# Kernel tuning notes

Measured on AMD Instinct MI355X. Metric: run time of the kernel, lower is better.

Reference implementation:

```python
import jax, jax.numpy as jnp
import numpy as np

HEADS = 4
DIM_HEAD = 32
DIM = 128
HIDDEN = HEADS * DIM_HEAD  # 128


def setup_inputs() -> dict:
    key = jax.random.key(0)
    k1, k2, k3, k4 = jax.random.split(key, 4)
    B, C, H, W = 8, DIM, 128, 128
    x = jax.random.normal(k1, (B, C, H, W), dtype=jnp.float32)
    # 1x1 conv weights stored as [out_ch, in_ch] (kernel dims squeezed)
    w_qkv = jax.random.normal(k2, (3 * HIDDEN, DIM), dtype=jnp.float32) * (1.0 / np.sqrt(DIM))
    w_out = jax.random.normal(k3, (DIM, HIDDEN), dtype=jnp.float32) * (1.0 / np.sqrt(HIDDEN))
    b_out = jax.random.normal(k4, (DIM,), dtype=jnp.float32) * 0.01
    return {"x": x, "w_qkv": w_qkv, "w_out": w_out, "b_out": b_out}


def reference(x, w_qkv, w_out, b_out):
    b, c, h, w = x.shape
    n = h * w
    # 1x1 conv == per-pixel matmul over channels
    qkv = jnp.einsum('bchw,oc->bohw', x, w_qkv)            # [b, 3*HIDDEN, h, w]
    # channel layout: (qkv, heads, dim_head)
    qkv = qkv.reshape(b, 3, HEADS, DIM_HEAD, n)            # [b, 3, H, d, n]
    q, k, v = qkv[:, 0], qkv[:, 1], qkv[:, 2]
    k = jax.nn.softmax(k, axis=-1)                         # softmax over spatial n
    context = jnp.einsum('bhdn,bhen->bhde', k, v)          # [b, H, d, d] (tiny)
    out = jnp.einsum('bhde,bhdn->bhen', context, q)        # [b, H, d, n]
    out = out.reshape(b, HIDDEN, h, w)
    y = jnp.einsum('bchw,oc->bohw', out, w_out) + b_out[None, :, None, None]
    return y
```

## Files before the change

kernel.cpp:

```cpp
#include <hip/hip_runtime.h>
#include <math.h>

#define C_ 128
#define N_ 16384

#define WS_Z    0
#define WS_CTX  1024
#define WS_BMAT 33792
#define WS_A    164864
#define WS_PCTX 295936
#define WS_PZ   (WS_PCTX + 1024*4096)
#define WS_END  (WS_PZ + 512*128)

typedef __attribute__((ext_vector_type(8))) short bf16x8;
typedef __attribute__((ext_vector_type(4))) float f32x4;
typedef __attribute__((ext_vector_type(4))) unsigned int u32x4;
typedef __attribute__((ext_vector_type(2))) unsigned int u32x2;

__device__ __forceinline__ unsigned int pkbf(float a, float b) {
  unsigned int r;
  asm("v_cvt_pk_bf16_f32 %0, %1, %2" : "=v"(r) : "v"(a), "v"(b));
  return r;
}

__device__ __forceinline__ bf16x8 make_frag(float4 u, float4 v) {
  u32x4 q = {pkbf(u.x, u.y), pkbf(u.z, u.w), pkbf(v.x, v.y), pkbf(v.z, v.w)};
  return *(bf16x8*)&q;
}

__device__ __forceinline__ bf16x8 lds_frag16(const unsigned short* p) {
  u32x4 q = *(const u32x4*)p;
  return *(bf16x8*)&q;
}

__device__ __forceinline__ void load4(const float* p, float* o) {
  float4 v = *(const float4*)p;
  o[0] = v.x; o[1] = v.y; o[2] = v.z; o[3] = v.w;
}

__device__ __forceinline__ void* xsa(void* base, int row, int col_bytes) {
  return (void*)((char*)base + row * 272 + (col_bytes ^ (((row >> 4) & 3) << 4)));
}

template<bool ATOMIC>
__global__ __launch_bounds__(512, 2) void k1_kv_ctx(const float* __restrict__ x,
                                                    const float* __restrict__ wqkv,
                                                    float* __restrict__ ws) {
  __shared__ __attribute__((aligned(16))) unsigned short xs[64][136];
  __shared__ __attribute__((aligned(16))) unsigned short ekv[2][128][72];
  const int tid  = threadIdx.x;
  const int wave = tid >> 6;
  const int l15  = tid & 15;
  const int l4   = (tid >> 4) & 3;
  const int b    = blockIdx.y;
  const int j    = blockIdx.x;
  const int h    = wave & 3;
  const int t    = wave >> 2;
  const int kvrow0 = h * 32 + t * 128;
  const float* xb = x + (size_t)b * ((size_t)C_ * N_);

  const int sn4 = tid & 15;
  const int scq = tid >> 4;

  bf16x8 wf[2][4];
  #pragma unroll
  for (int mi = 0; mi < 2; ++mi)
    #pragma unroll
    for (int ki = 0; ki < 4; ++ki) {
      const float* p = wqkv + (size_t)(128 + kvrow0 + mi * 16 + l15) * C_ + ki * 32 + l4 * 8;
      wf[mi][ki] = make_frag(*(const float4*)p, *(const float4*)(p + 4));
    }

  {
    float va[4][4];
    #pragma unroll
    for (int r = 0; r < 4; ++r)
      load4(xb + (size_t)(scq * 4 + r) * N_ + j * 256 + sn4 * 4, va[r]);
    #pragma unroll
    for (int i = 0; i < 4; ++i) {
      u32x2 w = {pkbf(va[0][i], va[1][i]), pkbf(va[2][i], va[3][i])};
      *(u32x2*)xsa(xs, sn4 * 4 + i, scq * 8) = w;
    }
  }
  __syncthreads();

  const f32x4 z4 = {0.f, 0.f, 0.f, 0.f};
  f32x4 ctxacc[2][2];
  #pragma unroll
  for (int i = 0; i < 2; ++i)
    #pragma unroll
    for (int jj = 0; jj < 2; ++jj) ctxacc[i][jj] = z4;
  float zacc[2] = {0.f, 0.f};

  for (int st = 0; st < 4; ++st) {
    float pf[4][4];
    if (st < 3) {
      const int nbn = j * 256 + (st + 1) * 64;
      #pragma unroll
      for (int r = 0; r < 4; ++r)
        load4(xb + (size_t)(scq * 4 + r) * N_ + nbn + sn4 * 4, pf[r]);
    }

    #pragma unroll
    for (int half = 0; half < 2; ++half) {
      f32x4 acc[2][2];
      #pragma unroll
      for (int a = 0; a < 2; ++a)
        #pragma unroll
        for (int m = 0; m < 2; ++m) acc[a][m] = z4;
      #pragma unroll
      for (int ki = 0; ki < 4; ++ki) {
        bf16x8 bfr[2];
        #pragma unroll
        for (int ni2 = 0; ni2 < 2; ++ni2)
          bfr[ni2] = lds_frag16((const unsigned short*)
              xsa(xs, half * 32 + ni2 * 16 + l15, ki * 64 + l4 * 16));
        #pragma unroll
        for (int ni2 = 0; ni2 < 2; ++ni2)
          #pragma unroll
          for (int mi = 0; mi < 2; ++mi)
            acc[ni2][mi] = __builtin_amdgcn_mfma_f32_16x16x32_bf16(
                bfr[ni2], wf[mi][ki], acc[ni2][mi], 0, 0, 0);
      }
      #pragma unroll
      for (int ni2 = 0; ni2 < 2; ++ni2)
        #pragma unroll
        for (int mi = 0; mi < 2; ++mi) {
          float e0, e1, e2, e3;
          if (t == 0) {
            e0 = __expf(acc[ni2][mi][0]); e1 = __expf(acc[ni2][mi][1]);
            e2 = __expf(acc[ni2][mi][2]); e3 = __expf(acc[ni2][mi][3]);
            zacc[mi] += (e0 + e1) + (e2 + e3);
          } else {
            e0 = acc[ni2][mi][0]; e1 = acc[ni2][mi][1];
            e2 = acc[ni2][mi][2]; e3 = acc[ni2][mi][3];
          }
          u32x2 w = {pkbf(e0, e1), pkbf(e2, e3)};
          *(u32x2*)&ekv[t][h * 32 + mi * 16 + l15][(half * 2 + ni2) * 16 + l4 * 4] = w;
        }
    }
    __syncthreads();

    {
      bf16x8 af2[2], bv2[2];
      #pragma unroll
      for (int m2 = 0; m2 < 2; ++m2)
        af2[m2] = lds_frag16(&ekv[0][h * 32 + m2 * 16 + l15][t * 32 + l4 * 8]);
      #pragma unroll
      for (int n2 = 0; n2 < 2; ++n2)
        bv2[n2] = lds_frag16(&ekv[1][h * 32 + n2 * 16 + l15][t * 32 + l4 * 8]);
      #pragma unroll
      for (int m2 = 0; m2 < 2; ++m2)
        #pragma unroll
        for (int n2 = 0; n2 < 2; ++n2)
          ctxacc[m2][n2] = __builtin_amdgcn_mfma_f32_16x16x32_bf16(
              af2[m2], bv2[n2], ctxacc[m2][n2], 0, 0, 0);
    }

    if (st < 3) {
      #pragma unroll
      for (int i = 0; i < 4; ++i) {
        u32x2 w = {pkbf(pf[0][i], pf[1][i]), pkbf(pf[2][i], pf[3][i])};
        *(u32x2*)xsa(xs, sn4 * 4 + i, scq * 8) = w;
      }
    }
    __syncthreads();
  }

  if (!ATOMIC) {
    float* ps = ws + WS_PCTX + (size_t)((b * 64 + j) * 2 + t) * 4096 + h * 1024;
    #pragma unroll
    for (int m2 = 0; m2 < 2; ++m2)
      #pragma unroll
      for (int n2 = 0; n2 < 2; ++n2)
        #pragma unroll
        for (int r = 0; r < 4; ++r)
          ps[(m2 * 16 + l4 * 4 + r) * 32 + n2 * 16 + l15] = ctxacc[m2][n2][r];
  } else {
    float* ctx = ws + WS_CTX + (size_t)(b * 4 + h) * 1024;
    #pragma unroll
    for (int m2 = 0; m2 < 2; ++m2)
      #pragma unroll
      for (int n2 = 0; n2 < 2; ++n2)
        #pragma unroll
        for (int r = 0; r < 4; ++r)
          atomicAdd(&ctx[(m2 * 16 + l4 * 4 + r) * 32 + n2 * 16 + l15],
                    ctxacc[m2][n2][r]);
  }
  if (t == 0) {
    #pragma unroll
    for (int mi = 0; mi < 2; ++mi) {
      float z = zacc[mi];
      z += __shfl_xor(z, 16);
      z += __shfl_xor(z, 32);
      if ((tid & 48) == 0) {
        int row = h * 32 + mi * 16 + l15;
        if (!ATOMIC)
          ws[WS_PZ + (size_t)(b * 64 + j) * 128 + row] = z;
        else
          atomicAdd(&ws[WS_Z + b * 128 + row], z);
      }
    }
  }
}

__global__ __launch_bounds__(256) void k1c(float* __restrict__ ws) {
  __shared__ float4 part[4][64];
  const int tid = threadIdx.x;
  const int eq = blockIdx.x;
  const int h  = blockIdx.y;
  const int b  = blockIdx.z;
  const int f4 = tid & 63;
  const int p  = tid >> 6;

  const float* base = ws + WS_PCTX + (size_t)(b * 128) * 4096
                         + h * 1024 + eq * 256 + f4 * 4;
  float4 s = {0.f, 0.f, 0.f, 0.f};
  #pragma unroll 8
  for (int q = 0; q < 32; ++q) {
    float4 v = *(const float4*)(base + (size_t)(p * 32 + q) * 4096);
    s.x += v.x; s.y += v.y; s.z += v.z; s.w += v.w;
  }
  part[p][f4] = s;

  if (eq == 0 && tid < 32) {
    const float* pz = ws + WS_PZ + (size_t)(b * 64) * 128 + h * 32 + tid;
    float z = 0.f;
    #pragma unroll 8
    for (int q = 0; q < 64; ++q) z += pz[(size_t)q * 128];
    ws[WS_Z + b * 128 + h * 32 + tid] = z;
  }
  __syncthreads();

  if (tid < 64) {
    float4 a = part[0][tid], c = part[1][tid], d = part[2][tid], e = part[3][tid];
    float4 o;
    o.x = (a.x + c.x) + (d.x + e.x);
    o.y = (a.y + c.y) + (d.y + e.y);
    o.z = (a.z + c.z) + (d.z + e.z);
    o.w = (a.w + c.w) + (d.w + e.w);
    *(float4*)(ws + WS_CTX + (size_t)(b * 4 + h) * 1024 + eq * 256 + tid * 4) = o;
  }
}

__global__ __launch_bounds__(256) void k2(const float* __restrict__ w_qkv,
                                          const float* __restrict__ w_out,
                                          float* __restrict__ ws) {
  __shared__ float bs[128][132];
  __shared__ float wqs[32][128];
  __shared__ float wos[32][132];
  __shared__ float cn[32][33];
  const int tid = threadIdx.x;
  const int oq = blockIdx.x, b = blockIdx.y;

  for (int h = 0; h < 4; ++h) {
    if (h) __syncthreads();
    const float* Z   = ws + WS_Z + b * 128 + h * 32;
    const float* ctx = ws + WS_CTX + ((b * 4 + h) * 32) * 32;
    #pragma unroll
    for (int k = 0; k < 4; ++k) {
      int idx = tid + k * 256;
      int d = idx >> 5, e = idx & 31;
      cn[d][e] = ctx[d * 32 + e] / Z[d];
    }
    #pragma unroll
    for (int k = 0; k < 4; ++k) {
      int idx = tid + k * 256;
      int d = idx >> 5, f4 = idx & 31;
      *(float4*)&wqs[d][f4 * 4] = *(const float4*)(w_qkv + (h * 32 + d) * 128 + f4 * 4);
    }
    __syncthreads();
    const int e = tid >> 3, cs = (tid & 7) * 16;
    float s[16];
    #pragma unroll
    for (int jj = 0; jj < 16; ++jj) s[jj] = 0.f;
    for (int d = 0; d < 32; ++d) {
      float v = cn[d][e];
      #pragma unroll
      for (int jj = 0; jj < 16; ++jj) s[jj] = fmaf(v, wqs[d][cs + jj], s[jj]);
    }
    #pragma unroll
    for (int jj = 0; jj < 16; ++jj) bs[h * 32 + e][cs + jj] = s[jj];
  }

  __syncthreads();
  #pragma unroll
  for (int k = 0; k < 4; ++k) {
    int idx = tid + k * 256;
    int r = idx >> 5, f4 = idx & 31;
    *(float4*)&wos[r][f4 * 4] = *(const float4*)(w_out + (oq * 32 + r) * 128 + f4 * 4);
  }
  __syncthreads();
  const int ol = tid >> 3, cq = (tid & 7) * 16;
  float s[16];
  #pragma unroll
  for (int jj = 0; jj < 16; ++jj) s[jj] = 0.f;
  for (int eg = 0; eg < 128; ++eg) {
    float w = wos[ol][eg];
    #pragma unroll
    for (int jj = 0; jj < 16; ++jj) s[jj] = fmaf(w, bs[eg][cq + jj], s[jj]);
  }
  float* A = ws + WS_A + ((size_t)b * 128 + oq * 32 + ol) * 128;
  #pragma unroll
  for (int jj = 0; jj < 16; ++jj) A[cq + jj] = s[jj];
}

__global__ __launch_bounds__(256, 2) void k3(const float* __restrict__ x,
                                             const float* __restrict__ bout,
                                             const float* __restrict__ ws,
                                             float* __restrict__ y) {
  __shared__ __attribute__((aligned(16))) unsigned short xs2[2][64][136];
  const int tid  = threadIdx.x;
  const int wave = tid >> 6;
  const int l15  = tid & 15;
  const int l4   = (tid >> 4) & 3;
  const int b    = blockIdx.y;
  const int n0   = blockIdx.x * 128;
  const float* xb = x + (size_t)b * ((size_t)C_ * N_);
  const float* A  = ws + WS_A + (size_t)b * 128 * 128;

  bf16x8 af[2][4];
  #pragma unroll
  for (int mi = 0; mi < 2; ++mi)
    #pragma unroll
    for (int ki = 0; ki < 4; ++ki) {
      const float* p = A + (size_t)(wave * 32 + mi * 16 + l15) * 128 + ki * 32 + l4 * 8;
      af[mi][ki] = make_frag(*(const float4*)p, *(const float4*)(p + 4));
    }
  float bias[2];
  #pragma unroll
  for (int mi = 0; mi < 2; ++mi) bias[mi] = bout[wave * 32 + mi * 16 + l15];

  #pragma unroll
  for (int it = 0; it < 2; ++it) {
    int idx = tid + it * 256;
    int n4 = idx & 15, cq = idx >> 4;
    float va[4][4];
    #pragma unroll
    for (int r = 0; r < 4; ++r)
      load4(xb + (size_t)(cq * 4 + r) * N_ + n0 + n4 * 4, va[r]);
    #pragma unroll
    for (int i = 0; i < 4; ++i) {
      u32x2 w = {pkbf(va[0][i], va[1][i]), pkbf(va[2][i], va[3][i])};
      *(u32x2*)xsa(&xs2[0][0][0], n4 * 4 + i, cq * 8) = w;
    }
  }
  __syncthreads();

  const f32x4 z4 = {0.f, 0.f, 0.f, 0.f};
  float* yb = y + (size_t)b * ((size_t)128 * N_);

  #pragma unroll
  for (int st = 0; st < 2; ++st) {
    const int nb = n0 + st * 64;
    f32x4 acc[4][2];
    #pragma unroll
    for (int ni = 0; ni < 4; ++ni)
      #pragma unroll
      for (int mi = 0; mi < 2; ++mi) acc[ni][mi] = z4;
    #pragma unroll
    for (int ki = 0; ki < 4; ++ki) {
      bf16x8 bfr[4];
      #pragma unroll
      for (int ni = 0; ni < 4; ++ni)
        bfr[ni] = lds_frag16((const unsigned short*)
            xsa(&xs2[st][0][0], ni * 16 + l15, ki * 64 + l4 * 16));
      #pragma unroll
      for (int ni = 0; ni < 4; ++ni)
        #pragma unroll
        for (int mi = 0; mi < 2; ++mi)
          acc[ni][mi] = __builtin_amdgcn_mfma_f32_16x16x32_bf16(
              bfr[ni], af[mi][ki], acc[ni][mi], 0, 0, 0);
    }

    if (st == 0) {
      #pragma unroll
      for (int it = 0; it < 2; ++it) {
        int idx = tid + it * 256;
        int n4 = idx & 15, cq = idx >> 4;
        float va[4][4];
        #pragma unroll
        for (int r = 0; r < 4; ++r)
          load4(xb + (size_t)(cq * 4 + r) * N_ + n0 + 64 + n4 * 4, va[r]);
        #pragma unroll
        for (int i = 0; i < 4; ++i) {
          u32x2 w = {pkbf(va[0][i], va[1][i]), pkbf(va[2][i], va[3][i])};
          *(u32x2*)xsa(&xs2[1][0][0], n4 * 4 + i, cq * 8) = w;
        }
      }
    }

    #pragma unroll
    for (int ni = 0; ni < 4; ++ni)
      #pragma unroll
      for (int mi = 0; mi < 2; ++mi) {
        float4 o;
        o.x = acc[ni][mi][0] + bias[mi];
        o.y = acc[ni][mi][1] + bias[mi];
        o.z = acc[ni][mi][2] + bias[mi];
        o.w = acc[ni][mi][3] + bias[mi];
        *(float4*)(yb + (size_t)(wave * 32 + mi * 16 + l15) * N_ + nb + ni * 16 + l4 * 4) = o;
      }

    if (st == 0) __syncthreads();
  }
}

extern "C" void kernel_launch(void* const* d_in, const int* in_sizes, int n_in,
                              void* d_out, int out_size, void* d_ws, size_t ws_size,
                              hipStream_t stream) {
  const float* x     = (const float*)d_in[0];
  const float* w_qkv = (const float*)d_in[1];
  const float* w_out = (const float*)d_in[2];
  const float* b_out = (const float*)d_in[3];
  float* y  = (float*)d_out;
  float* ws = (float*)d_ws;

  const bool partial = ws_size >= (size_t)WS_END * sizeof(float);
  if (partial) {
    k1_kv_ctx<false><<<dim3(64, 8), 512, 0, stream>>>(x, w_qkv, ws);
    k1c<<<dim3(4, 4, 8), 256, 0, stream>>>(ws);
  } else {
    hipMemsetAsync(ws, 0, (1024 + 32768) * sizeof(float), stream);
    k1_kv_ctx<true><<<dim3(64, 8), 512, 0, stream>>>(x, w_qkv, ws);
  }
  k2<<<dim3(4, 8), 256, 0, stream>>>(w_qkv, w_out, ws);
  k3<<<dim3(128, 8), 256, 0, stream>>>(x, b_out, ws, y);
}
```

Measured before the change: 77.84 us.

## Restructure output projection kernel to 512 threads with double-buffered x pipeline

```diff
diff --git a/kernel.cpp b/kernel.cpp
--- a/kernel.cpp
+++ b/kernel.cpp
@@ -115,12 +115,14 @@
         for (int ni2 = 0; ni2 < 2; ++ni2)
           bfr[ni2] = lds_frag16((const unsigned short*)
               xsa(xs, half * 32 + ni2 * 16 + l15, ki * 64 + l4 * 16));
+        __builtin_amdgcn_s_setprio(1);
         #pragma unroll
         for (int ni2 = 0; ni2 < 2; ++ni2)
           #pragma unroll
           for (int mi = 0; mi < 2; ++mi)
             acc[ni2][mi] = __builtin_amdgcn_mfma_f32_16x16x32_bf16(
                 bfr[ni2], wf[mi][ki], acc[ni2][mi], 0, 0, 0);
+        __builtin_amdgcn_s_setprio(0);
       }
       #pragma unroll
       for (int ni2 = 0; ni2 < 2; ++ni2)
@@ -149,12 +151,14 @@
       #pragma unroll
       for (int n2 = 0; n2 < 2; ++n2)
         bv2[n2] = lds_frag16(&ekv[1][h * 32 + n2 * 16 + l15][t * 32 + l4 * 8]);
+      __builtin_amdgcn_s_setprio(1);
       #pragma unroll
       for (int m2 = 0; m2 < 2; ++m2)
         #pragma unroll
         for (int n2 = 0; n2 < 2; ++n2)
           ctxacc[m2][n2] = __builtin_amdgcn_mfma_f32_16x16x32_bf16(
               af2[m2], bv2[n2], ctxacc[m2][n2], 0, 0, 0);
+      __builtin_amdgcn_s_setprio(0);
     }
 
     if (st < 3) {
@@ -305,7 +309,7 @@
   for (int jj = 0; jj < 16; ++jj) A[cq + jj] = s[jj];
 }
 
-__global__ __launch_bounds__(256, 2) void k3(const float* __restrict__ x,
+__global__ __launch_bounds__(512, 2) void k3(const float* __restrict__ x,
                                              const float* __restrict__ bout,
                                              const float* __restrict__ ws,
                                              float* __restrict__ y) {
@@ -315,34 +319,30 @@
   const int l15  = tid & 15;
   const int l4   = (tid >> 4) & 3;
   const int b    = blockIdx.y;
-  const int n0   = blockIdx.x * 128;
+  const int n0   = blockIdx.x * 256;
   const float* xb = x + (size_t)b * ((size_t)C_ * N_);
   const float* A  = ws + WS_A + (size_t)b * 128 * 128;
 
-  bf16x8 af[2][4];
-  #pragma unroll
-  for (int mi = 0; mi < 2; ++mi)
-    #pragma unroll
-    for (int ki = 0; ki < 4; ++ki) {
-      const float* p = A + (size_t)(wave * 32 + mi * 16 + l15) * 128 + ki * 32 + l4 * 8;
-      af[mi][ki] = make_frag(*(const float4*)p, *(const float4*)(p + 4));
-    }
-  float bias[2];
-  #pragma unroll
-  for (int mi = 0; mi < 2; ++mi) bias[mi] = bout[wave * 32 + mi * 16 + l15];
-
-  #pragma unroll
-  for (int it = 0; it < 2; ++it) {
-    int idx = tid + it * 256;
-    int n4 = idx & 15, cq = idx >> 4;
+  const int sn4 = tid & 15;
+  const int scq = tid >> 4;
+
+  bf16x8 af[4];
+  #pragma unroll
+  for (int ki = 0; ki < 4; ++ki) {
+    const float* p = A + (size_t)(wave * 16 + l15) * 128 + ki * 32 + l4 * 8;
+    af[ki] = make_frag(*(const float4*)p, *(const float4*)(p + 4));
+  }
+  const float bias = bout[wave * 16 + l15];
+
+  {
     float va[4][4];
     #pragma unroll
     for (int r = 0; r < 4; ++r)
-      load4(xb + (size_t)(cq * 4 + r) * N_ + n0 + n4 * 4, va[r]);
+      load4(xb + (size_t)(scq * 4 + r) * N_ + n0 + sn4 * 4, va[r]);
     #pragma unroll
     for (int i = 0; i < 4; ++i) {
       u32x2 w = {pkbf(va[0][i], va[1][i]), pkbf(va[2][i], va[3][i])};
-      *(u32x2*)xsa(&xs2[0][0][0], n4 * 4 + i, cq * 8) = w;
+      *(u32x2*)xsa(&xs2[0][0][0], sn4 * 4 + i, scq * 8) = w;
     }
   }
   __syncthreads();
@@ -350,59 +350,50 @@
   const f32x4 z4 = {0.f, 0.f, 0.f, 0.f};
   float* yb = y + (size_t)b * ((size_t)128 * N_);
 
-  #pragma unroll
-  for (int st = 0; st < 2; ++st) {
+  for (int st = 0; st < 4; ++st) {
     const int nb = n0 + st * 64;
-    f32x4 acc[4][2];
-    #pragma unroll
-    for (int ni = 0; ni < 4; ++ni)
-      #pragma unroll
-      for (int mi = 0; mi < 2; ++mi) acc[ni][mi] = z4;
+
+    float pf[4][4];
+    if (st < 3) {
+      #pragma unroll
+      for (int r = 0; r < 4; ++r)
+        load4(xb + (size_t)(scq * 4 + r) * N_ + nb + 64 + sn4 * 4, pf[r]);
+    }
+
+    f32x4 acc[4];
+    #pragma unroll
+    for (int ni = 0; ni < 4; ++ni) acc[ni] = z4;
     #pragma unroll
     for (int ki = 0; ki < 4; ++ki) {
       bf16x8 bfr[4];
       #pragma unroll
       for (int ni = 0; ni < 4; ++ni)
         bfr[ni] = lds_frag16((const unsigned short*)
-            xsa(&xs2[st][0][0], ni * 16 + l15, ki * 64 + l4 * 16));
+            xsa(&xs2[st & 1][0][0], ni * 16 + l15, ki * 64 + l4 * 16));
       #pragma unroll
       for (int ni = 0; ni < 4; ++ni)
-        #pragma unroll
-        for (int mi = 0; mi < 2; ++mi)
-          acc[ni][mi] = __builtin_amdgcn_mfma_f32_16x16x32_bf16(
-              bfr[ni], af[mi][ki], acc[ni][mi], 0, 0, 0);
-    }
-
-    if (st == 0) {
-      #pragma unroll
-      for (int it = 0; it < 2; ++it) {
-        int idx = tid + it * 256;
-        int n4 = idx & 15, cq = idx >> 4;
-        float va[4][4];
-        #pragma unroll
-        for (int r = 0; r < 4; ++r)
-          load4(xb + (size_t)(cq * 4 + r) * N_ + n0 + 64 + n4 * 4, va[r]);
-        #pragma unroll
-        for (int i = 0; i < 4; ++i) {
-          u32x2 w = {pkbf(va[0][i], va[1][i]), pkbf(va[2][i], va[3][i])};
-          *(u32x2*)xsa(&xs2[1][0][0], n4 * 4 + i, cq * 8) = w;
-        }
+        acc[ni] = __builtin_amdgcn_mfma_f32_16x16x32_bf16(
+            bfr[ni], af[ki], acc[ni], 0, 0, 0);
+    }
+
+    #pragma unroll
+    for (int ni = 0; ni < 4; ++ni) {
+      float4 o;
+      o.x = acc[ni][0] + bias;
+      o.y = acc[ni][1] + bias;
+      o.z = acc[ni][2] + bias;
+      o.w = acc[ni][3] + bias;
+      *(float4*)(yb + (size_t)(wave * 16 + l15) * N_ + nb + ni * 16 + l4 * 4) = o;
+    }
+
+    if (st < 3) {
+      #pragma unroll
+      for (int i = 0; i < 4; ++i) {
+        u32x2 w = {pkbf(pf[0][i], pf[1][i]), pkbf(pf[2][i], pf[3][i])};
+        *(u32x2*)xsa(&xs2[(st + 1) & 1][0][0], sn4 * 4 + i, scq * 8) = w;
       }
-    }
-
-    #pragma unroll
-    for (int ni = 0; ni < 4; ++ni)
-      #pragma unroll
-      for (int mi = 0; mi < 2; ++mi) {
-        float4 o;
-        o.x = acc[ni][mi][0] + bias[mi];
-        o.y = acc[ni][mi][1] + bias[mi];
-        o.z = acc[ni][mi][2] + bias[mi];
-        o.w = acc[ni][mi][3] + bias[mi];
-        *(float4*)(yb + (size_t)(wave * 32 + mi * 16 + l15) * N_ + nb + ni * 16 + l4 * 4) = o;
-      }
-
-    if (st == 0) __syncthreads();
+      __syncthreads();
+    }
   }
 }
 
@@ -425,5 +416,5 @@
     k1_kv_ctx<true><<<dim3(64, 8), 512, 0, stream>>>(x, w_qkv, ws);
   }
   k2<<<dim3(4, 8), 256, 0, stream>>>(w_qkv, w_out, ws);
-  k3<<<dim3(128, 8), 256, 0, stream>>>(x, b_out, ws, y);
-}
+  k3<<<dim3(64, 8), 512, 0, stream>>>(x, b_out, ws, y);
+}
```

Result: faster. 75.25 us (-3.3%).
